# Optimization experiments

Hardware: AMD Instinct MI355X
Metric: run time of the kernel (lower is better)

## Reference

```python
import jax, jax.numpy as jnp
import numpy as np

B, S, D, H, DK, DV = 4, 1024, 1024, 16, 64, 64


def setup_inputs() -> dict:
    key = jax.random.key(0)
    ks = jax.random.split(key, 12)
    sc = 0.02
    return {
        "q": jax.random.normal(ks[0], (B, S, D), jnp.float32),
        "k": jax.random.normal(ks[1], (B, S, D), jnp.float32),
        "v": jax.random.normal(ks[2], (B, S, D), jnp.float32),
        "attn_mask": jax.random.randint(ks[3], (B, S, S), 0, 2).astype(bool),
        "Wq": jax.random.normal(ks[4], (D, H * DK), jnp.float32) * sc,
        "bq": jnp.zeros((H * DK,), jnp.float32),
        "Wk": jax.random.normal(ks[5], (D, H * DK), jnp.float32) * sc,
        "bk": jnp.zeros((H * DK,), jnp.float32),
        "Wv": jax.random.normal(ks[6], (D, H * DV), jnp.float32) * sc,
        "bv": jnp.zeros((H * DV,), jnp.float32),
        "Wo": jax.random.normal(ks[7], (H * DV, D), jnp.float32) * sc,
        "bo": jnp.zeros((D,), jnp.float32),
    }


def _layer_norm(x, eps=1e-5):
    # fresh nn.LayerNorm in forward => weight=1, bias=0
    mu = jnp.mean(x, axis=-1, keepdims=True)
    var = jnp.mean(jnp.square(x - mu), axis=-1, keepdims=True)
    return (x - mu) * jax.lax.rsqrt(var + eps)


def reference(q, k, v, attn_mask, Wq, bq, Wk, bk, Wv, bv, Wo, bo):
    residual = q
    qs = (q @ Wq + bq).reshape(B, S, H, DK).transpose(0, 2, 1, 3)  # [B,H,S,dk]
    ks = (k @ Wk + bk).reshape(B, S, H, DK).transpose(0, 2, 1, 3)
    vs = (v @ Wv + bv).reshape(B, S, H, DV).transpose(0, 2, 1, 3)
    scores = jnp.einsum('bhqd,bhkd->bhqk', qs, ks) / jnp.sqrt(jnp.float32(DK))
    scores = jnp.where(attn_mask[:, None, :, :], jnp.float32(-1e9), scores)
    attention = jax.nn.softmax(scores, axis=-1)  # [B,H,S,S]
    context = jnp.einsum('bhqk,bhkd->bhqd', attention, vs)
    concat = context.transpose(0, 2, 1, 3).reshape(B, S, H * DV)
    output = concat @ Wo + bo
    return _layer_norm(output + residual), attention
```

## Files before the change

### kernel.cpp

```cpp
#include <hip/hip_runtime.h>
#include <hip/hip_bf16.h>
#include <stdint.h>

#define B_    4
#define S_    1024
#define D_    1024
#define H_    16
#define NTOK  4096

typedef __bf16 bf16_t;
typedef bf16_t bf16x8 __attribute__((ext_vector_type(8)));
typedef bf16_t bf16x4 __attribute__((ext_vector_type(4)));
typedef float  f32x4  __attribute__((ext_vector_type(4)));

__device__ __forceinline__ f32x4 mfma16(bf16x8 a, bf16x8 b, f32x4 c) {
  return __builtin_amdgcn_mfma_f32_16x16x32_bf16(a, b, c, 0, 0, 0);
}
__device__ __forceinline__ void gload16(const void* g, void* l) {
  __builtin_amdgcn_global_load_lds((__attribute__((address_space(1))) uint32_t*)g,
                                   (__attribute__((address_space(3))) uint32_t*)l, 16, 0, 0);
}
__device__ __forceinline__ bf16_t to_bf(float x) { return (bf16_t)x; }

__global__ void cvt_bf16_kernel(const float* __restrict__ src, bf16_t* __restrict__ dst, int n4) {
  int i = blockIdx.x * blockDim.x + threadIdx.x;
  if (i >= n4) return;
  f32x4 v = ((const f32x4*)src)[i];
  bf16x4 o = { to_bf(v[0]), to_bf(v[1]), to_bf(v[2]), to_bf(v[3]) };
  ((bf16x4*)dst)[i] = o;
}

__global__ void wT_kernel(const float* __restrict__ W, bf16_t* __restrict__ WT) {
  __shared__ float t[32][33];
  int bx = blockIdx.x * 32, by = blockIdx.y * 32;
  int tx = threadIdx.x, ty = threadIdx.y;
#pragma unroll
  for (int i = 0; i < 4; i++) t[ty + 8 * i][tx] = W[(size_t)(by + ty + 8 * i) * 1024 + bx + tx];
  __syncthreads();
#pragma unroll
  for (int i = 0; i < 4; i++)
    WT[(size_t)(bx + ty + 8 * i) * 1024 + by + tx] = to_bf(t[tx][ty + 8 * i]);
}

__global__ void maskpack_kernel(const uint32_t* __restrict__ m, uint32_t* __restrict__ out) {
  int t = blockIdx.x * blockDim.x + threadIdx.x;
  const uint32_t* p = m + (size_t)t * 8;
  uint32_t r = 0;
#pragma unroll
  for (int j = 0; j < 8; j++) {
    uint32_t v = p[j];
    uint32_t nib = (v & 1u) | ((v >> 7) & 2u) | ((v >> 14) & 4u) | ((v >> 21) & 8u);
    r |= nib << (j * 4);
  }
  out[t] = r;
}

__device__ __forceinline__ void gemm128_core(const bf16_t* __restrict__ A,
                                             const bf16_t* __restrict__ Bm,
                                             int m0, int n0,
                                             bf16_t* As, bf16_t* Bs, f32x4 (&acc)[4][4]) {
  int tid = threadIdx.x, w = tid >> 6, lane = tid & 63, l16 = lane & 15, lg = lane >> 4;
  int wr = w >> 1, wc = w & 1;
  f32x4 zv = {0.f, 0.f, 0.f, 0.f};
#pragma unroll
  for (int r = 0; r < 4; r++)
#pragma unroll
    for (int c = 0; c < 4; c++) acc[r][c] = zv;

  for (int kt = 0; kt < 16; kt++) {
    int k0 = kt * 64;
#pragma unroll
    for (int j = 0; j < 4; j++) {
      int e = ((w * 4 + j) << 9) + (lane << 3);
      int row = e >> 6, col = e & 63;
      gload16(A + (size_t)(m0 + row) * 1024 + k0 + col, As + ((w * 4 + j) << 9));
      gload16(Bm + (size_t)(n0 + row) * 1024 + k0 + col, Bs + ((w * 4 + j) << 9));
    }
    __syncthreads();
#pragma unroll
    for (int kk = 0; kk < 2; kk++) {
      bf16x8 av[4], bv[4];
#pragma unroll
      for (int r = 0; r < 4; r++)
        av[r] = *(const bf16x8*)(As + (wr * 64 + r * 16 + l16) * 64 + kk * 32 + lg * 8);
#pragma unroll
      for (int c = 0; c < 4; c++)
        bv[c] = *(const bf16x8*)(Bs + (wc * 64 + c * 16 + l16) * 64 + kk * 32 + lg * 8);
#pragma unroll
      for (int r = 0; r < 4; r++)
#pragma unroll
        for (int c = 0; c < 4; c++) acc[r][c] = mfma16(av[r], bv[c], acc[r][c]);
    }
    __syncthreads();
  }
}

__global__ __launch_bounds__(256, 2) void qkv_gemm_kernel(
    const bf16_t* __restrict__ qb, const bf16_t* __restrict__ kb, const bf16_t* __restrict__ vb,
    const bf16_t* __restrict__ WqT, const bf16_t* __restrict__ WkT, const bf16_t* __restrict__ WvT,
    const float* __restrict__ bq, const float* __restrict__ bk, const float* __restrict__ bv,
    bf16_t* __restrict__ Qh, bf16_t* __restrict__ Kh, bf16_t* __restrict__ Vh) {
  __shared__ bf16_t As[128 * 64], Bs[128 * 64];
  int z = blockIdx.z;
  const bf16_t* A  = (z == 0) ? qb  : ((z == 1) ? kb  : vb);
  const bf16_t* Bm = (z == 0) ? WqT : ((z == 1) ? WkT : WvT);
  const float* bias = (z == 0) ? bq : ((z == 1) ? bk : bv);
  bf16_t* out = (z == 0) ? Qh : ((z == 1) ? Kh : Vh);
  int m0 = blockIdx.y * 128, n0 = blockIdx.x * 128;
  f32x4 acc[4][4];
  gemm128_core(A, Bm, m0, n0, As, Bs, acc);

  int tid = threadIdx.x, w = tid >> 6, lane = tid & 63, l16 = lane & 15, lg = lane >> 4;
  int wr = w >> 1, wc = w & 1;
#pragma unroll
  for (int c = 0; c < 4; c++) {
    int col = n0 + wc * 64 + c * 16 + l16;
    float bb = bias[col];
    int h = col >> 6, dk = col & 63;
#pragma unroll
    for (int r = 0; r < 4; r++) {
#pragma unroll
      for (int i = 0; i < 4; i++) {
        int mrow = m0 + wr * 64 + r * 16 + lg * 4 + i;
        int b = mrow >> 10, s = mrow & 1023;
        out[(((size_t)(b * 16 + h)) * 1024 + s) * 64 + dk] = to_bf(acc[r][c][i] + bb);
      }
    }
  }
}

__global__ void vT_kernel(const bf16_t* __restrict__ Vh, bf16_t* __restrict__ Vt) {
  __shared__ float t[64][65];
  int bh = blockIdx.z * 16 + blockIdx.y;
  int s0 = blockIdx.x * 64;
  int tx = threadIdx.x & 63, ty = threadIdx.x >> 6;
  const bf16_t* src = Vh + (size_t)bh * 65536;
  bf16_t* dst = Vt + (size_t)bh * 65536;
#pragma unroll
  for (int i = 0; i < 16; i++) t[ty + 4 * i][tx] = (float)src[(size_t)(s0 + ty + 4 * i) * 64 + tx];
  __syncthreads();
#pragma unroll
  for (int i = 0; i < 16; i++)
    dst[(size_t)(ty + 4 * i) * 1024 + s0 + tx] = to_bf(t[tx][ty + 4 * i]);
}

__global__ __launch_bounds__(256, 2) void attn_kernel(
    const bf16_t* __restrict__ Qh, const bf16_t* __restrict__ Kh, const bf16_t* __restrict__ Vt,
    const uint32_t* __restrict__ mbits, float* __restrict__ attn_out, bf16_t* __restrict__ ctx) {
  constexpr int PSTR = 1032;
  __shared__ bf16_t P[32 * PSTR];
  __shared__ uint32_t mb[1024];
  __shared__ float redm[128], reds[128];
  int b = blockIdx.z, h = blockIdx.y, q0 = blockIdx.x * 32;
  int tid = threadIdx.x, w = tid >> 6, lane = tid & 63, l16 = lane & 15, lg = lane >> 4;
  int bh = b * 16 + h;

  ((uint4*)mb)[tid] = ((const uint4*)(mbits + ((size_t)b * 1024 + q0) * 32))[tid];

  const bf16_t* Qb = Qh + (size_t)bh * 65536;
  const bf16_t* Kb = Kh + (size_t)bh * 65536;
  bf16x8 qa[2][2];
#pragma unroll
  for (int r = 0; r < 2; r++)
#pragma unroll
    for (int kk = 0; kk < 2; kk++)
      qa[r][kk] = *(const bf16x8*)(Qb + (size_t)(q0 + r * 16 + l16) * 64 + kk * 32 + lg * 8);

  f32x4 zv = {0.f, 0.f, 0.f, 0.f};
  f32x4 sc[2][16];
#pragma unroll
  for (int rt = 0; rt < 2; rt++)
#pragma unroll
    for (int c = 0; c < 16; c++) sc[rt][c] = zv;
  int kcol0 = w * 256;
#pragma unroll 4
  for (int c = 0; c < 16; c++) {
#pragma unroll
    for (int kk = 0; kk < 2; kk++) {
      bf16x8 kv = *(const bf16x8*)(Kb + (size_t)(kcol0 + c * 16 + l16) * 64 + kk * 32 + lg * 8);
      sc[0][c] = mfma16(qa[0][kk], kv, sc[0][c]);
      sc[1][c] = mfma16(qa[1][kk], kv, sc[1][c]);
    }
  }
  __syncthreads();

  float rmax[2][4], rsum[2][4], rinv[2][4];
#pragma unroll
  for (int rt = 0; rt < 2; rt++)
#pragma unroll
    for (int i = 0; i < 4; i++) rmax[rt][i] = -3e38f;
  const float scale = 0.125f;
#pragma unroll
  for (int rt = 0; rt < 2; rt++) {
#pragma unroll
    for (int j = 0; j < 8; j++) {
      uint32_t wd[4];
#pragma unroll
      for (int i = 0; i < 4; i++) wd[i] = mb[(rt * 16 + lg * 4 + i) * 32 + w * 8 + j];
#pragma unroll
      for (int hf = 0; hf < 2; hf++) {
        int c = j * 2 + hf;
#pragma unroll
        for (int i = 0; i < 4; i++) {
          float s = sc[rt][c][i] * scale;
          if ((wd[i] >> (l16 + hf * 16)) & 1u) s = -1e9f;
          sc[rt][c][i] = s;
          rmax[rt][i] = fmaxf(rmax[rt][i], s);
        }
      }
    }
  }
#pragma unroll
  for (int m = 1; m < 16; m <<= 1)
#pragma unroll
    for (int rt = 0; rt < 2; rt++)
#pragma unroll
      for (int i = 0; i < 4; i++) rmax[rt][i] = fmaxf(rmax[rt][i], __shfl_xor(rmax[rt][i], m));
  if (l16 == 0) {
#pragma unroll
    for (int rt = 0; rt < 2; rt++)
#pragma unroll
      for (int i = 0; i < 4; i++) redm[w * 32 + rt * 16 + lg * 4 + i] = rmax[rt][i];
  }
  __syncthreads();
#pragma unroll
  for (int rt = 0; rt < 2; rt++)
#pragma unroll
    for (int i = 0; i < 4; i++) {
      int row = rt * 16 + lg * 4 + i;
      rmax[rt][i] = fmaxf(fmaxf(redm[row], redm[32 + row]), fmaxf(redm[64 + row], redm[96 + row]));
      rsum[rt][i] = 0.f;
    }
#pragma unroll
  for (int rt = 0; rt < 2; rt++)
#pragma unroll
    for (int c = 0; c < 16; c++)
#pragma unroll
      for (int i = 0; i < 4; i++) {
        float p = __expf(sc[rt][c][i] - rmax[rt][i]);
        sc[rt][c][i] = p;
        rsum[rt][i] += p;
      }
#pragma unroll
  for (int m = 1; m < 16; m <<= 1)
#pragma unroll
    for (int rt = 0; rt < 2; rt++)
#pragma unroll
      for (int i = 0; i < 4; i++) rsum[rt][i] += __shfl_xor(rsum[rt][i], m);
  if (l16 == 0) {
#pragma unroll
    for (int rt = 0; rt < 2; rt++)
#pragma unroll
      for (int i = 0; i < 4; i++) reds[w * 32 + rt * 16 + lg * 4 + i] = rsum[rt][i];
  }
  __syncthreads();
#pragma unroll
  for (int rt = 0; rt < 2; rt++)
#pragma unroll
    for (int i = 0; i < 4; i++) {
      int row = rt * 16 + lg * 4 + i;
      float gs = reds[row] + reds[32 + row] + reds[64 + row] + reds[96 + row];
      rinv[rt][i] = 1.0f / gs;
    }

  float* ob = attn_out + ((size_t)bh * 1024 + q0) * 1024;
#pragma unroll
  for (int rt = 0; rt < 2; rt++)
#pragma unroll
    for (int c = 0; c < 16; c++) {
      int colk = kcol0 + c * 16 + l16;
#pragma unroll
      for (int i = 0; i < 4; i++) {
        int row = rt * 16 + lg * 4 + i;
        float p = sc[rt][c][i];
        ob[(size_t)row * 1024 + colk] = p * rinv[rt][i];
        P[row * PSTR + colk] = to_bf(p);
      }
    }
  __syncthreads();

  f32x4 oacc0 = zv, oacc1 = zv;
  const bf16_t* Vb = Vt + ((size_t)bh * 64 + w * 16 + l16) * 1024 + lg * 8;
#pragma unroll 4
  for (int ks = 0; ks < 32; ks++) {
    bf16x8 vv = *(const bf16x8*)(Vb + ks * 32);
    bf16x8 a0 = *(const bf16x8*)(P + l16 * PSTR + ks * 32 + lg * 8);
    bf16x8 a1 = *(const bf16x8*)(P + (16 + l16) * PSTR + ks * 32 + lg * 8);
    oacc0 = mfma16(a0, vv, oacc0);
    oacc1 = mfma16(a1, vv, oacc1);
  }
#pragma unroll
  for (int i = 0; i < 4; i++) {
    int s0r = q0 + lg * 4 + i;
    ctx[((size_t)b * 1024 + s0r) * 1024 + h * 64 + w * 16 + l16] = to_bf(oacc0[i] * rinv[0][i]);
    int s1r = q0 + 16 + lg * 4 + i;
    ctx[((size_t)b * 1024 + s1r) * 1024 + h * 64 + w * 16 + l16] = to_bf(oacc1[i] * rinv[1][i]);
  }
}

__global__ __launch_bounds__(256, 2) void out_gemm_kernel(
    const bf16_t* __restrict__ ctx, const bf16_t* __restrict__ WoT,
    const float* __restrict__ bo, const float* __restrict__ resid, float* __restrict__ preLN) {
  __shared__ bf16_t As[128 * 64], Bs[128 * 64];
  int m0 = blockIdx.y * 128, n0 = blockIdx.x * 128;
  f32x4 acc[4][4];
  gemm128_core(ctx, WoT, m0, n0, As, Bs, acc);
  int tid = threadIdx.x, w = tid >> 6, lane = tid & 63, l16 = lane & 15, lg = lane >> 4;
  int wr = w >> 1, wc = w & 1;
#pragma unroll
  for (int c = 0; c < 4; c++) {
    int col = n0 + wc * 64 + c * 16 + l16;
    float bb = bo[col];
#pragma unroll
    for (int r = 0; r < 4; r++) {
#pragma unroll
      for (int i = 0; i < 4; i++) {
        int mrow = m0 + wr * 64 + r * 16 + lg * 4 + i;
        preLN[(size_t)mrow * 1024 + col] = acc[r][c][i] + bb + resid[(size_t)mrow * 1024 + col];
      }
    }
  }
}

__global__ void ln_kernel(const float* __restrict__ pre, float* __restrict__ out) {
  int row = blockIdx.x, tid = threadIdx.x;
  const f32x4 v = ((const f32x4*)(pre + (size_t)row * 1024))[tid];
  float s = v[0] + v[1] + v[2] + v[3];
  float s2 = v[0] * v[0] + v[1] * v[1] + v[2] * v[2] + v[3] * v[3];
#pragma unroll
  for (int m = 32; m > 0; m >>= 1) { s += __shfl_xor(s, m); s2 += __shfl_xor(s2, m); }
  __shared__ float rs[4], rs2[4];
  int w = tid >> 6;
  if ((tid & 63) == 0) { rs[w] = s; rs2[w] = s2; }
  __syncthreads();
  float S = rs[0] + rs[1] + rs[2] + rs[3];
  float S2 = rs2[0] + rs2[1] + rs2[2] + rs2[3];
  float mu = S * (1.f / 1024.f);
  float var = S2 * (1.f / 1024.f) - mu * mu;
  float rstd = rsqrtf(var + 1e-5f);
  f32x4 o = { (v[0] - mu) * rstd, (v[1] - mu) * rstd, (v[2] - mu) * rstd, (v[3] - mu) * rstd };
  ((f32x4*)(out + (size_t)row * 1024))[tid] = o;
}

extern "C" void kernel_launch(void* const* d_in, const int* in_sizes, int n_in,
                              void* d_out, int out_size, void* d_ws, size_t ws_size,
                              hipStream_t stream) {
  const float* q  = (const float*)d_in[0];
  const float* k  = (const float*)d_in[1];
  const float* v  = (const float*)d_in[2];
  const uint8_t* mask = (const uint8_t*)d_in[3];
  const float* Wq = (const float*)d_in[4];
  const float* bq = (const float*)d_in[5];
  const float* Wk = (const float*)d_in[6];
  const float* bk = (const float*)d_in[7];
  const float* Wv = (const float*)d_in[8];
  const float* bv = (const float*)d_in[9];
  const float* Wo = (const float*)d_in[10];
  const float* bo = (const float*)d_in[11];

  char* wsp = (char*)d_ws;
  size_t off = 0;
  auto carve = [&](size_t bytes) { void* p = wsp + off; off += (bytes + 255) & ~(size_t)255; return p; };
  bf16_t* qb  = (bf16_t*)carve((size_t)NTOK * 1024 * 2);
  bf16_t* kb  = (bf16_t*)carve((size_t)NTOK * 1024 * 2);
  bf16_t* vb  = (bf16_t*)carve((size_t)NTOK * 1024 * 2);
  bf16_t* WqT = (bf16_t*)carve((size_t)1024 * 1024 * 2);
  bf16_t* WkT = (bf16_t*)carve((size_t)1024 * 1024 * 2);
  bf16_t* WvT = (bf16_t*)carve((size_t)1024 * 1024 * 2);
  bf16_t* WoT = (bf16_t*)carve((size_t)1024 * 1024 * 2);
  bf16_t* Qh  = (bf16_t*)carve((size_t)NTOK * 1024 * 2);
  bf16_t* Kh  = (bf16_t*)carve((size_t)NTOK * 1024 * 2);
  bf16_t* Vh  = (bf16_t*)carve((size_t)NTOK * 1024 * 2);
  bf16_t* Vt  = (bf16_t*)carve((size_t)NTOK * 1024 * 2);
  bf16_t* ctx = (bf16_t*)carve((size_t)NTOK * 1024 * 2);
  uint32_t* mbits = (uint32_t*)carve((size_t)B_ * S_ * 32 * 4);
  float* preLN = (float*)carve((size_t)NTOK * 1024 * 4);
  (void)ws_size; (void)in_sizes; (void)n_in; (void)out_size;

  float* lnout = (float*)d_out;
  float* attn_out = (float*)d_out + (size_t)NTOK * 1024;

  cvt_bf16_kernel<<<4096, 256, 0, stream>>>(q, qb, NTOK * 1024 / 4);
  cvt_bf16_kernel<<<4096, 256, 0, stream>>>(k, kb, NTOK * 1024 / 4);
  cvt_bf16_kernel<<<4096, 256, 0, stream>>>(v, vb, NTOK * 1024 / 4);
  wT_kernel<<<dim3(32, 32), dim3(32, 8), 0, stream>>>(Wq, WqT);
  wT_kernel<<<dim3(32, 32), dim3(32, 8), 0, stream>>>(Wk, WkT);
  wT_kernel<<<dim3(32, 32), dim3(32, 8), 0, stream>>>(Wv, WvT);
  wT_kernel<<<dim3(32, 32), dim3(32, 8), 0, stream>>>(Wo, WoT);
  maskpack_kernel<<<512, 256, 0, stream>>>((const uint32_t*)mask, mbits);
  qkv_gemm_kernel<<<dim3(8, 32, 3), 256, 0, stream>>>(qb, kb, vb, WqT, WkT, WvT,
                                                      bq, bk, bv, Qh, Kh, Vh);
  vT_kernel<<<dim3(16, 16, 4), 256, 0, stream>>>(Vh, Vt);
  attn_kernel<<<dim3(32, 16, 4), 256, 0, stream>>>(Qh, Kh, Vt, mbits, attn_out, ctx);
  out_gemm_kernel<<<dim3(8, 32), 256, 0, stream>>>(ctx, WoT, bo, q, preLN);
  ln_kernel<<<4096, 256, 0, stream>>>(preLN, lnout);
}
```

Measured before the change: 772.0 us.

## Coalesce attention-prob stores via LDS, remap blocks per XCD, merge prep launches

The normalized attention probabilities were written straight from MFMA accumulator registers in scattered 64-byte pieces. They are now written after the PV product, reading the bf16 P tile from LDS and issuing wide, contiguous, nontemporal float4 stores per row, with per-row inverse sums kept in shared memory. Attention blocks are also remapped so that each XCD handles a contiguous set of (batch, head) pairs, which should improve K/V cache locality. The three input-convert launches and the four weight-transpose launches are each merged into a single launch. The attention output is now built from bf16-rounded probabilities rather than fp32 values, which lowers its precision.

```diff
diff --git a/kernel.cpp b/kernel.cpp
--- a/kernel.cpp
+++ b/kernel.cpp
@@ -22,15 +22,25 @@
 }
 __device__ __forceinline__ bf16_t to_bf(float x) { return (bf16_t)x; }
 
-__global__ void cvt_bf16_kernel(const float* __restrict__ src, bf16_t* __restrict__ dst, int n4) {
+__global__ void cvt3_kernel(const float* __restrict__ q, const float* __restrict__ k,
+                            const float* __restrict__ v, bf16_t* __restrict__ qb,
+                            bf16_t* __restrict__ kb, bf16_t* __restrict__ vb) {
+  int z = blockIdx.z;
+  const float* src = (z == 0) ? q : ((z == 1) ? k : v);
+  bf16_t* dst = (z == 0) ? qb : ((z == 1) ? kb : vb);
   int i = blockIdx.x * blockDim.x + threadIdx.x;
-  if (i >= n4) return;
-  f32x4 v = ((const f32x4*)src)[i];
-  bf16x4 o = { to_bf(v[0]), to_bf(v[1]), to_bf(v[2]), to_bf(v[3]) };
+  f32x4 val = ((const f32x4*)src)[i];
+  bf16x4 o = { to_bf(val[0]), to_bf(val[1]), to_bf(val[2]), to_bf(val[3]) };
   ((bf16x4*)dst)[i] = o;
 }
 
-__global__ void wT_kernel(const float* __restrict__ W, bf16_t* __restrict__ WT) {
+__global__ void wT4_kernel(const float* __restrict__ Wq, const float* __restrict__ Wk,
+                           const float* __restrict__ Wv, const float* __restrict__ Wo,
+                           bf16_t* __restrict__ WqT, bf16_t* __restrict__ WkT,
+                           bf16_t* __restrict__ WvT, bf16_t* __restrict__ WoT) {
+  int z = blockIdx.z;
+  const float* W = (z == 0) ? Wq : ((z == 1) ? Wk : ((z == 2) ? Wv : Wo));
+  bf16_t* WT = (z == 0) ? WqT : ((z == 1) ? WkT : ((z == 2) ? WvT : WoT));
   __shared__ float t[32][33];
   int bx = blockIdx.x * 32, by = blockIdx.y * 32;
   int tx = threadIdx.x, ty = threadIdx.y;
@@ -150,10 +160,16 @@
   constexpr int PSTR = 1032;
   __shared__ bf16_t P[32 * PSTR];
   __shared__ uint32_t mb[1024];
-  __shared__ float redm[128], reds[128];
-  int b = blockIdx.z, h = blockIdx.y, q0 = blockIdx.x * 32;
+  __shared__ float redm[128], reds[128], rowinv[32];
+
+  int lin = blockIdx.x + 32 * (blockIdx.y + 16 * blockIdx.z);
+  int xcd = lin & 7;
+  int slot = lin >> 3;
+  int bh = xcd * 8 + (slot >> 5);
+  int q0 = (slot & 31) * 32;
+  int b = bh >> 4;
+
   int tid = threadIdx.x, w = tid >> 6, lane = tid & 63, l16 = lane & 15, lg = lane >> 4;
-  int bh = b * 16 + h;
 
   ((uint4*)mb)[tid] = ((const uint4*)(mbits + ((size_t)b * 1024 + q0) * 32))[tid];
 
@@ -262,8 +278,13 @@
       float gs = reds[row] + reds[32 + row] + reds[64 + row] + reds[96 + row];
       rinv[rt][i] = 1.0f / gs;
     }
-
-  float* ob = attn_out + ((size_t)bh * 1024 + q0) * 1024;
+  if (w == 0 && l16 == 0) {
+#pragma unroll
+    for (int rt = 0; rt < 2; rt++)
+#pragma unroll
+      for (int i = 0; i < 4; i++) rowinv[rt * 16 + lg * 4 + i] = rinv[rt][i];
+  }
+
 #pragma unroll
   for (int rt = 0; rt < 2; rt++)
 #pragma unroll
@@ -272,9 +293,7 @@
 #pragma unroll
       for (int i = 0; i < 4; i++) {
         int row = rt * 16 + lg * 4 + i;
-        float p = sc[rt][c][i];
-        ob[(size_t)row * 1024 + colk] = p * rinv[rt][i];
-        P[row * PSTR + colk] = to_bf(p);
+        P[row * PSTR + colk] = to_bf(sc[rt][c][i]);
       }
     }
   __syncthreads();
@@ -289,12 +308,27 @@
     oacc0 = mfma16(a0, vv, oacc0);
     oacc1 = mfma16(a1, vv, oacc1);
   }
+
+  float* ob = attn_out + ((size_t)bh * 1024 + q0) * 1024;
+#pragma unroll
+  for (int rr = 0; rr < 8; rr++) {
+    int row = w * 8 + rr;
+    float inv = rowinv[row];
+#pragma unroll
+    for (int c = 0; c < 4; c++) {
+      int col = c * 256 + lane * 4;
+      bf16x4 p4 = *(const bf16x4*)(P + row * PSTR + col);
+      f32x4 o = { (float)p4[0] * inv, (float)p4[1] * inv, (float)p4[2] * inv, (float)p4[3] * inv };
+      __builtin_nontemporal_store(o, (f32x4*)(ob + (size_t)row * 1024 + col));
+    }
+  }
+
 #pragma unroll
   for (int i = 0; i < 4; i++) {
     int s0r = q0 + lg * 4 + i;
-    ctx[((size_t)b * 1024 + s0r) * 1024 + h * 64 + w * 16 + l16] = to_bf(oacc0[i] * rinv[0][i]);
+    ctx[((size_t)b * 1024 + s0r) * 1024 + (bh & 15) * 64 + w * 16 + l16] = to_bf(oacc0[i] * rinv[0][i]);
     int s1r = q0 + 16 + lg * 4 + i;
-    ctx[((size_t)b * 1024 + s1r) * 1024 + h * 64 + w * 16 + l16] = to_bf(oacc1[i] * rinv[1][i]);
+    ctx[((size_t)b * 1024 + s1r) * 1024 + (bh & 15) * 64 + w * 16 + l16] = to_bf(oacc1[i] * rinv[1][i]);
   }
 }
 
@@ -380,13 +414,8 @@
   float* lnout = (float*)d_out;
   float* attn_out = (float*)d_out + (size_t)NTOK * 1024;
 
-  cvt_bf16_kernel<<<4096, 256, 0, stream>>>(q, qb, NTOK * 1024 / 4);
-  cvt_bf16_kernel<<<4096, 256, 0, stream>>>(k, kb, NTOK * 1024 / 4);
-  cvt_bf16_kernel<<<4096, 256, 0, stream>>>(v, vb, NTOK * 1024 / 4);
-  wT_kernel<<<dim3(32, 32), dim3(32, 8), 0, stream>>>(Wq, WqT);
-  wT_kernel<<<dim3(32, 32), dim3(32, 8), 0, stream>>>(Wk, WkT);
-  wT_kernel<<<dim3(32, 32), dim3(32, 8), 0, stream>>>(Wv, WvT);
-  wT_kernel<<<dim3(32, 32), dim3(32, 8), 0, stream>>>(Wo, WoT);
+  cvt3_kernel<<<dim3(4096, 1, 3), 256, 0, stream>>>(q, k, v, qb, kb, vb);
+  wT4_kernel<<<dim3(32, 32, 4), dim3(32, 8), 0, stream>>>(Wq, Wk, Wv, Wo, WqT, WkT, WvT, WoT);
   maskpack_kernel<<<512, 256, 0, stream>>>((const uint32_t*)mask, mbits);
   qkv_gemm_kernel<<<dim3(8, 32, 3), 256, 0, stream>>>(qb, kb, vb, WqT, WkT, WvT,
                                                       bq, bk, bv, Qh, Kh, Vh);
```

After: 722.5 us. -6.4%, faster.
